# Performance work log

Hardware: AMD Instinct MI355X
Metric: run time of the kernel (lower is better)

Reference implementation:

```python
import jax, jax.numpy as jnp
import numpy as np
from jax import lax

EPS_BN = 1e-5
EPS_LN = 1e-5
K = 16  # patch size (cubic)
S = 8   # patch stride (cubic)


def _conv3d(x, w, stride):
    # x: [B,C,D,H,W], w: [O,I,kD,kH,kW], padding=1 on all spatial dims (torch padding=1)
    return lax.conv_general_dilated(
        x, w, (stride, stride, stride), [(1, 1), (1, 1), (1, 1)],
        dimension_numbers=('NCDHW', 'OIDHW', 'NCDHW'))


def _bn_relu(x, g, b):
    # train-mode BatchNorm3d: batch statistics over (B, D, H, W) per channel
    mean = jnp.mean(x, axis=(0, 2, 3, 4), keepdims=True)
    var = jnp.var(x, axis=(0, 2, 3, 4), keepdims=True)
    xh = (x - mean) * lax.rsqrt(var + EPS_BN)
    g = g[None, :, None, None, None]
    b = b[None, :, None, None, None]
    return jax.nn.relu(xh * g + b)


def _extract_patches_3d(f0):
    # f0: [B,C,D,H,W] -> patches [B,N,C*K^3] (C-major then kD,kH,kW, matching torch unfold),
    # coords [B,N,3]
    B, C, D, H, W = f0.shape
    Do, Ho, Wo = (D - K) // S + 1, (H - K) // S + 1, (W - K) // S + 1
    di = jnp.arange(Do)[:, None] * S + jnp.arange(K)[None, :]  # [Do,K]
    hi = jnp.arange(Ho)[:, None] * S + jnp.arange(K)[None, :]
    wi = jnp.arange(Wo)[:, None] * S + jnp.arange(K)[None, :]
    p = f0[:, :, di]                 # [B,C,Do,K,H,W]
    p = p[:, :, :, :, hi]            # [B,C,Do,K,Ho,K,W]
    p = p[:, :, :, :, :, :, wi]      # [B,C,Do,K,Ho,K,Wo,K]
    p = p.transpose(0, 2, 4, 6, 1, 3, 5, 7)  # [B,Do,Ho,Wo,C,K,K,K]
    patches = p.reshape(B, Do * Ho * Wo, C * K * K * K)
    half = (K - 1) / 2.0
    z = (jnp.arange(Do) * S + half) / max(D - 1, 1)
    y = (jnp.arange(Ho) * S + half) / max(H - 1, 1)
    xg = (jnp.arange(Wo) * S + half) / max(W - 1, 1)
    zz, yy, xx = jnp.meshgrid(z, y, xg, indexing='ij')
    coords = jnp.stack([zz.reshape(-1), yy.reshape(-1), xx.reshape(-1)], axis=-1)
    coords = jnp.broadcast_to(coords[None], (B,) + coords.shape)
    return patches, coords


def _layer_norm(x, g, b):
    mu = jnp.mean(x, axis=-1, keepdims=True)
    var = jnp.var(x, axis=-1, keepdims=True)
    return (x - mu) * lax.rsqrt(var + EPS_LN) * g + b


def setup_inputs() -> dict:
    key = jax.random.key(0)
    ks = jax.random.split(key, 8)
    C_in, mid, stem, tok_d, aux_d = 1, 16, 32, 128, 32
    pdim = stem * K * K * K  # 131072
    f32 = jnp.float32
    x = jax.random.normal(ks[0], (2, C_in, 128, 128, 128), dtype=f32)
    def kinit(k, shape, fan_in):
        return jax.random.normal(k, shape, dtype=f32) * (1.0 / np.sqrt(fan_in))
    return {
        'x': x,
        'conv1_w': kinit(ks[1], (mid, C_in, 3, 3, 3), C_in * 27),
        'bn1_g': jnp.ones((mid,), f32), 'bn1_b': jnp.zeros((mid,), f32),
        'conv2_w': kinit(ks[2], (mid, mid, 3, 3, 3), mid * 27),
        'bn2_g': jnp.ones((mid,), f32), 'bn2_b': jnp.zeros((mid,), f32),
        'conv3_w': kinit(ks[3], (stem, mid, 3, 3, 3), mid * 27),
        'bn3_g': jnp.ones((stem,), f32), 'bn3_b': jnp.zeros((stem,), f32),
        'tok_w': kinit(ks[4], (tok_d, pdim), pdim), 'tok_b': jnp.zeros((tok_d,), f32),
        'aux_w': kinit(ks[5], (aux_d, pdim), pdim), 'aux_b': jnp.zeros((aux_d,), f32),
        'ln_g': jnp.ones((tok_d,), f32), 'ln_b': jnp.zeros((tok_d,), f32),
    }


def reference(x, conv1_w, bn1_g, bn1_b, conv2_w, bn2_g, bn2_b, conv3_w, bn3_g, bn3_b,
              tok_w, tok_b, aux_w, aux_b, ln_g, ln_b):
    f0 = _bn_relu(_conv3d(x, conv1_w, 1), bn1_g, bn1_b)
    f0 = _bn_relu(_conv3d(f0, conv2_w, 1), bn2_g, bn2_b)
    f0 = _bn_relu(_conv3d(f0, conv3_w, 2), bn3_g, bn3_b)  # [B,32,64,64,64]
    patches, coords = _extract_patches_3d(f0)  # [B,N,131072]
    tokens = jnp.einsum('bnp,tp->bnt', patches, tok_w) + tok_b
    tokens = _layer_norm(tokens, ln_g, ln_b)
    aux = jnp.einsum('bnp,ap->bna', patches, aux_w) + aux_b
    return tokens, aux, coords
```

## Files before the change

### kernel.cpp

```cpp
#include <hip/hip_runtime.h>
#include <hip/hip_bf16.h>


typedef __hip_bfloat16 bf16;
typedef __attribute__((ext_vector_type(8))) short short8;
typedef __attribute__((ext_vector_type(4))) float f32x4;
__device__ __forceinline__ float b2f(bf16 v){ return __bfloat162float(v); }
__device__ __forceinline__ bf16 f2b(float v){ return __float2bfloat16(v); }
__device__ __forceinline__ unsigned short f2bu(float f){
  unsigned u = __float_as_uint(f);
  return (unsigned short)((u + 0x7fff + ((u>>16)&1)) >> 16);
}

#define SP12 2097152
#define SP3  262144
#define M_TOT 686
#define TOK_OFF 0
#define AUX_OFF 87808
#define CRD_OFF 109760
#define KSPLIT 32
#define NSLAB 32

__global__ __launch_bounds__(256) void k_packw(const float* __restrict__ w1,
                                               const float* __restrict__ w2,
                                               const float* __restrict__ w3,
                                               unsigned short* __restrict__ wp1,
                                               unsigned short* __restrict__ wp2,
                                               unsigned short* __restrict__ wp3){
  int i = blockIdx.x*256 + threadIdx.x;
  if(i < 512){
    int oc = i>>5, k = i&31;
    float v = (k<27)? w1[oc*27+k] : 0.f;
    wp1[i] = f2bu(v);
  } else if(i < 7680){
    int j = i - 512;
    int oc = j/448, k = j - oc*448;
    int tap = k>>4, ic = k&15;
    float v = (tap<27)? w2[(oc*16+ic)*27+tap] : 0.f;
    wp2[oc*448+k] = f2bu(v);
  } else if(i < 22016){
    int j = i - 7680;
    int oc = j/448, k = j - oc*448;
    int tap = k>>4, ic = k&15;
    float v = (tap<27)? w3[(oc*16+ic)*27+tap] : 0.f;
    wp3[oc*448+k] = f2bu(v);
  }
}

#define C1P 88
__global__ __launch_bounds__(256) void k_conv1(const float* __restrict__ x,
                                               const unsigned short* __restrict__ wp1,
                                               unsigned short* __restrict__ y1u,
                                               float* __restrict__ psum){
  __shared__ unsigned short in_l[6*6*C1P];
  int t = threadIdx.x;
  int bx = blockIdx.x;
  int xt = bx&1, yt = (bx>>1)&31, zt = (bx>>6)&31, b = bx>>11;
  int x0 = xt*64, y0 = yt*4, z0 = zt*4;

  for(int i=t; i<648; i+=256){
    int c = i%18; int row = i/18; int yy = row%6; int zz = row/6;
    int gz = z0-1+zz, gy = y0-1+yy;
    bool rowok = ((unsigned)gz<128u) && ((unsigned)gy<128u);
    int gx4 = x0-4+c*4;
    const float* rp = x + (size_t)b*SP12 + (rowok? ((gz<<14)+(gy<<7)) : 0);
    float v0,v1,v2,v3;
    if(rowok && gx4>=0 && gx4<=124){
      float4 v = *(const float4*)(rp + gx4);
      v0=v.x; v1=v.y; v2=v.z; v3=v.w;
    } else {
      float vv[4];
#pragma unroll
      for(int e=0;e<4;e++){
        int gx = gx4+e; bool ok = rowok && ((unsigned)gx<128u);
        float val = rp[ok? gx : 0];
        vv[e] = ok? val : 0.f;
      }
      v0=vv[0]; v1=vv[1]; v2=vv[2]; v3=vv[3];
    }
    uint2 p;
    p.x = (unsigned)f2bu(v0) | ((unsigned)f2bu(v1)<<16);
    p.y = (unsigned)f2bu(v2) | ((unsigned)f2bu(v3)<<16);
    *(uint2*)&in_l[row*C1P + c*4] = p;
  }
  __syncthreads();

  int lane = t&63, w = t>>6;
  int m = lane&15, q = lane>>4;
  short8 bfr = *(const short8*)(wp1 + m*32 + q*8);
  int toff[8];
#pragma unroll
  for(int j=0;j<8;j++){
    int tap = q*8+j; if(tap>26) tap=26;
    int dz = tap/9; int rr = tap-dz*9; int dy = rr/3; int dx = rr-dy*3;
    toff[j] = (dz*6+dy)*C1P + dx + 3 + m;
  }
  float s=0.f, qv=0.f;
#pragma unroll
  for(int yi=0; yi<4; yi++){
#pragma unroll
    for(int mg=0; mg<4; mg++){
      int base = (w*6+yi)*C1P + mg*16;
      short8 af;
#pragma unroll
      for(int j=0;j<8;j++) af[j] = (short)in_l[base + toff[j]];
      f32x4 acc = (f32x4){0.f,0.f,0.f,0.f};
      acc = __builtin_amdgcn_mfma_f32_16x16x32_bf16(af, bfr, acc, 0,0,0);
      int gz = z0+w, gy = y0+yi, gxb = x0 + mg*16 + q*4;
      size_t vbase = (size_t)((b<<21)|(gz<<14)|(gy<<7)|gxb);
      unsigned short* dst = y1u + vbase*16 + m;
#pragma unroll
      for(int reg=0; reg<4; reg++){
        float v = acc[reg];
        s += v; qv += v*v;
        dst[reg*16] = f2bu(v);
      }
    }
  }
  s  += __shfl_xor(s,16);  s  += __shfl_xor(s,32);
  qv += __shfl_xor(qv,16); qv += __shfl_xor(qv,32);
  __syncthreads();
  float* red = (float*)in_l;
  if(lane<16){ red[w*32+lane]=s; red[w*32+16+lane]=qv; }
  __syncthreads();
  if(t<32){
    float tot = red[t]+red[32+t]+red[64+t]+red[96+t];
    atomicAdd(&psum[(blockIdx.x & (NSLAB-1))*64 + t], tot);
  }
}

__global__ void k_finalize(const float* __restrict__ psum, const float* __restrict__ g,
                           const float* __restrict__ bb, float* __restrict__ scsh,
                           int C, float invN){
  int i = threadIdx.x;
  if(i<C){
    float s=0.f, q=0.f;
    for(int sl=0; sl<NSLAB; sl++){ s += psum[sl*64+i]; q += psum[sl*64+C+i]; }
    float mean = s*invN;
    float var  = q*invN - mean*mean;
    float sc = g[i]*rsqrtf(var+1e-5f);
    scsh[i]   = sc;
    scsh[C+i] = bb[i] - mean*sc;
  }
}

__global__ __launch_bounds__(256) void k_conv2(const unsigned short* __restrict__ y1u,
                                               const unsigned short* __restrict__ wp2,
                                               const float* __restrict__ scsh,
                                               unsigned short* __restrict__ y2u,
                                               float* __restrict__ psum2){
  __shared__ unsigned short tile[10*6*18*16];
  __shared__ float s_sc[16], s_sh[16];
  int t = threadIdx.x;
  if(t < 32){ float v = scsh[t]; if(t<16) s_sc[t]=v; else s_sh[t-16]=v; }
  __syncthreads();
  int bx = blockIdx.x;
  int txx = bx&7, tyy=(bx>>3)&31, tzz=(bx>>8)&15, b=bx>>12;
  int x0 = txx*16, y0 = tyy*4, z0 = tzz*8;
  for(int i=t;i<2160;i+=256){
    int vox = i>>1, h = i&1;
    int xl_ = vox%18; int r1 = vox/18; int yy_ = r1%6; int zz_ = r1/6;
    int gx = x0+xl_-1, gy = y0+yy_-1, gz = z0+zz_-1;
    bool ok = ((unsigned)gx<128u)&&((unsigned)gy<128u)&&((unsigned)gz<128u);
    uint4 o; o.x=0;o.y=0;o.z=0;o.w=0;
    if(ok){
      uint4 u = *(const uint4*)(y1u + ((size_t)((b<<21)|(gz<<14)|(gy<<7)|gx))*16 + h*8);
      int c0 = h*8;
      unsigned uu[4]; uu[0]=u.x; uu[1]=u.y; uu[2]=u.z; uu[3]=u.w;
      unsigned oo[4];
#pragma unroll
      for(int j=0;j<4;j++){
        float lo = fmaxf(__uint_as_float(uu[j]<<16)        *s_sc[c0+2*j]   + s_sh[c0+2*j],   0.f);
        float hi = fmaxf(__uint_as_float(uu[j]&0xffff0000u)*s_sc[c0+2*j+1] + s_sh[c0+2*j+1], 0.f);
        oo[j] = (unsigned)f2bu(lo) | ((unsigned)f2bu(hi)<<16);
      }
      o.x=oo[0]; o.y=oo[1]; o.z=oo[2]; o.w=oo[3];
    }
    int sw = (xl_>>2)&1;
    *(uint4*)&tile[vox*16 + ((h^sw)*8)] = o;
  }
  __syncthreads();

  int lane = t & 63, wid = t>>6;
  int m = lane & 15, q = lane>>4;
  int qh = q&1, qt = q>>1;
  f32x4 acc[8];
#pragma unroll
  for(int r=0;r<8;r++) acc[r] = (f32x4){0.f,0.f,0.f,0.f};
  const char* tbase = (const char*)tile + wid*6912;
  const unsigned short* wrow = wp2 + m*448 + q*8;
#pragma unroll
  for(int kp=0;kp<14;kp++){
    short8 bfr = *(const short8*)(wrow + kp*32);
    int tap = kp*2 + qt; if(tap>26) tap=26;
    int dz = tap/9; int rr = tap - dz*9; int dy = rr/3; int dx = rr - dy*3;
    int xl = m + dx;
    int abyte = ((dz*6 + dy)*18 + xl)*32 + ((qh ^ ((xl>>2)&1))*16);
    const char* ap = tbase + abyte;
#pragma unroll
    for(int r=0;r<8;r++){
      const short8 af = *(const short8*)(ap + ((r>>2)*6 + (r&3))*576);
      acc[r] = __builtin_amdgcn_mfma_f32_16x16x32_bf16(af, bfr, acc[r], 0,0,0);
    }
  }
  float s=0.f, qv=0.f;
#pragma unroll
  for(int r=0;r<8;r++){
    int gz = z0 + wid*2 + (r>>2), gy = y0 + (r&3);
    size_t vbase = (size_t)((b<<21)|(gz<<14)|(gy<<7)) + x0 + q*4;
#pragma unroll
    for(int reg=0;reg<4;reg++){
      float v = acc[r][reg];
      s += v; qv += v*v;
      y2u[(vbase+reg)*16 + m] = f2bu(v);
    }
  }
  s  += __shfl_xor(s,16);  s  += __shfl_xor(s,32);
  qv += __shfl_xor(qv,16); qv += __shfl_xor(qv,32);
  __syncthreads();
  float* red = (float*)tile;
  if(lane<16){ red[wid*32+lane]=s; red[wid*32+16+lane]=qv; }
  __syncthreads();
  if(t<32){
    float tot = red[t]+red[32+t]+red[64+t]+red[96+t];
    atomicAdd(&psum2[(blockIdx.x & (NSLAB-1))*64 + t], tot);
  }
}

__global__ __launch_bounds__(256) void k_conv3(const unsigned short* __restrict__ y2u,
                                               const unsigned short* __restrict__ wp3,
                                               const float* __restrict__ scsh,
                                               bf16* __restrict__ f0,
                                               float* __restrict__ psum3){
  __shared__ unsigned short tile3[5*9*33*16];
  __shared__ float s_sc[16], s_sh[16];
  int t = threadIdx.x;
  if(t < 32){ float v = scsh[t]; if(t<16) s_sc[t]=v; else s_sh[t-16]=v; }
  __syncthreads();
  int bx = blockIdx.x;
  int tx = bx&3, ty=(bx>>2)&15, tz=(bx>>6)&31, b=bx>>11;
  int x0 = tx*16, y0 = ty*4, z0 = tz*2;
  int gx0 = 2*x0-1, gy0 = 2*y0-1, gz0 = 2*z0-1;
  for(int i=t;i<2970;i+=256){
    int vox = i>>1, h = i&1;
    int xl_ = vox%33; int r1 = vox/33; int yy_ = r1%9; int zz_ = r1/9;
    int gx = gx0+xl_, gy = gy0+yy_, gz = gz0+zz_;
    bool ok = (gx>=0)&&(gy>=0)&&(gz>=0);
    uint4 o; o.x=0;o.y=0;o.z=0;o.w=0;
    if(ok){
      uint4 u = *(const uint4*)(y2u + ((size_t)((b<<21)|(gz<<14)|(gy<<7)|gx))*16 + h*8);
      int c0 = h*8;
      unsigned uu[4]; uu[0]=u.x; uu[1]=u.y; uu[2]=u.z; uu[3]=u.w;
      unsigned oo[4];
#pragma unroll
      for(int j=0;j<4;j++){
        float lo = fmaxf(__uint_as_float(uu[j]<<16)        *s_sc[c0+2*j]   + s_sh[c0+2*j],   0.f);
        float hi = fmaxf(__uint_as_float(uu[j]&0xffff0000u)*s_sc[c0+2*j+1] + s_sh[c0+2*j+1], 0.f);
        oo[j] = (unsigned)f2bu(lo) | ((unsigned)f2bu(hi)<<16);
      }
      o.x=oo[0]; o.y=oo[1]; o.z=oo[2]; o.w=oo[3];
    }
    int sw = (xl_>>2)&1;
    *(uint4*)&tile3[vox*16 + ((h^sw)*8)] = o;
  }
  __syncthreads();

  int lane = t & 63, wid = t>>6;
  int m = lane & 15, q = lane>>4;
  int qh = q&1, qt = q>>1;
  f32x4 acc[2][2];
#pragma unroll
  for(int r=0;r<2;r++){ acc[r][0]=(f32x4){0,0,0,0}; acc[r][1]=(f32x4){0,0,0,0}; }
  const unsigned short* wrow0 = wp3 + m*448 + q*8;
  const unsigned short* wrow1 = wp3 + (16+m)*448 + q*8;
#pragma unroll
  for(int kp=0;kp<14;kp++){
    short8 bf0 = *(const short8*)(wrow0 + kp*32);
    short8 bf1 = *(const short8*)(wrow1 + kp*32);
    int tap = kp*2 + qt; if(tap>26) tap=26;
    int dz = tap/9; int rr = tap - dz*9; int dy = rr/3; int dx = rr - dy*3;
    int xl = 2*m + dx;
    int hb = (qh ^ ((xl>>2)&1))*16;
#pragma unroll
    for(int rl=0;rl<2;rl++){
      int row = wid*2 + rl;
      int tz_ = 2*(row>>2) + dz;
      int ty_ = 2*(row&3) + dy;
      const short8 af = *(const short8*)((const char*)tile3 + ((tz_*9+ty_)*33 + xl)*32 + hb);
      acc[rl][0] = __builtin_amdgcn_mfma_f32_16x16x32_bf16(af, bf0, acc[rl][0], 0,0,0);
      acc[rl][1] = __builtin_amdgcn_mfma_f32_16x16x32_bf16(af, bf1, acc[rl][1], 0,0,0);
    }
  }
  float s0=0.f,q0=0.f,s1=0.f,q1=0.f;
#pragma unroll
  for(int rl=0;rl<2;rl++){
    int row = wid*2 + rl;
    int oz = z0 + (row>>2), oy = y0 + (row&3);
    size_t sp = (size_t)oz*4096 + oy*64 + x0 + q*4;
#pragma unroll
    for(int oct=0;oct<2;oct++){
      int oc = oct*16 + m;
      bf16* dst = f0 + (size_t)(b*32+oc)*SP3 + sp;
#pragma unroll
      for(int reg=0;reg<4;reg++){
        float v = acc[rl][oct][reg];
        if(oct==0){ s0 += v; q0 += v*v; } else { s1 += v; q1 += v*v; }
        dst[reg] = f2b(v);
      }
    }
  }
  s0 += __shfl_xor(s0,16); s0 += __shfl_xor(s0,32);
  q0 += __shfl_xor(q0,16); q0 += __shfl_xor(q0,32);
  s1 += __shfl_xor(s1,16); s1 += __shfl_xor(s1,32);
  q1 += __shfl_xor(q1,16); q1 += __shfl_xor(q1,32);
  __syncthreads();
  float* red = (float*)tile3;
  if(lane<16){
    red[wid*64+lane]    = s0; red[wid*64+16+lane] = s1;
    red[wid*64+32+lane] = q0; red[wid*64+48+lane] = q1;
  }
  __syncthreads();
  if(t<64){
    float tot = red[t]+red[64+t]+red[128+t]+red[192+t];
    atomicAdd(&psum3[(blockIdx.x & (NSLAB-1))*64 + t], tot);
  }
}

__global__ __launch_bounds__(256) void k_cvtw(const float* __restrict__ tokw,
                                              const float* __restrict__ auxw,
                                              unsigned short* __restrict__ wb){
  int i = blockIdx.x*256 + threadIdx.x;
  int n = i >> 15;
  int g = i & 32767;
  const float* src = (n<128)? tokw + (size_t)n*131072 : auxw + (size_t)(n-128)*131072;
  float4 v = *(const float4*)(src + g*4);
  ushort4 o; o.x=f2bu(v.x); o.y=f2bu(v.y); o.z=f2bu(v.z); o.w=f2bu(v.w);
  *(ushort4*)(wb + (size_t)n*131072 + g*4) = o;
}

__global__ __launch_bounds__(256) void k_gemm(const bf16* __restrict__ f0,
                                              const unsigned short* __restrict__ wb,
                                              const float* __restrict__ scsh3,
                                              float* __restrict__ out_acc){
  __shared__ unsigned short Al[64*72];
  __shared__ unsigned short Wl[160*72];
  int mblk = blockIdx.x % 11; int ks = blockIdx.x / 11;
  int M0 = mblk*64;
  int c  = ks;
  float sc = scsh3[c], sh = scsh3[32+c];
  int t = threadIdx.x;
  int lane = t & 63; int wid = t >> 6;
  int wm = (wid & 1)*32; int wn = (wid >> 1)*80;
  f32x4 acc[2][5];
#pragma unroll
  for(int i=0;i<2;i++)
#pragma unroll
    for(int j=0;j<5;j++) acc[i][j] = (f32x4){0.f,0.f,0.f,0.f};

  int ky_off0 = (t&7)>>1, half0 = t&1;
  int m_a = t>>3;
  int mg1 = M0 + m_a;       if(mg1>685) mg1=685;
  int mg2 = M0 + m_a + 32;  if(mg2>685) mg2=685;
  int b1 = mg1/343, r1 = mg1%343;
  int b2 = mg2/343, r2 = mg2%343;
  int sp1 = ((r1/49)*8)*4096 + (((r1/7)%7)*8)*64 + (r1%7)*8;
  int sp2 = ((r2/49)*8)*4096 + (((r2/7)%7)*8)*64 + (r2%7)*8;
  const bf16* f0c1 = f0 + (size_t)(b1*32+c)*SP3;
  const bf16* f0c2 = f0 + (size_t)(b2*32+c)*SP3;

  for(int bk=0; bk<64; bk++){
    int kz = bk>>2; int kyb = (bk&3)*4;
    __syncthreads();
#pragma unroll
    for(int p=0;p<5;p++){
      int n = p*32 + (t>>3);
      int koff = (t&7)*8;
      uint4 v = *(const uint4*)(wb + (size_t)n*131072 + ks*4096 + bk*64 + koff);
      *(uint4*)&Wl[n*72 + koff] = v;
    }
    {
      int ky = kyb + ky_off0; int xo = half0*8;
      int ldso = ky_off0*16 + half0*8;
      uint4 u1 = *(const uint4*)(f0c1 + sp1 + kz*4096 + ky*64 + xo);
      uint4 u2 = *(const uint4*)(f0c2 + sp2 + kz*4096 + ky*64 + xo);
      unsigned uu[8]; uu[0]=u1.x; uu[1]=u1.y; uu[2]=u1.z; uu[3]=u1.w;
      uu[4]=u2.x; uu[5]=u2.y; uu[6]=u2.z; uu[7]=u2.w;
      unsigned outw[8];
#pragma unroll
      for(int qq=0;qq<8;qq++){
        float lo = fmaxf(__uint_as_float(uu[qq]<<16)*sc + sh, 0.f);
        float hi = fmaxf(__uint_as_float(uu[qq]&0xffff0000u)*sc + sh, 0.f);
        outw[qq] = (unsigned)f2bu(lo) | ((unsigned)f2bu(hi)<<16);
      }
      uint4 w1; w1.x=outw[0]; w1.y=outw[1]; w1.z=outw[2]; w1.w=outw[3];
      uint4 w2; w2.x=outw[4]; w2.y=outw[5]; w2.z=outw[6]; w2.w=outw[7];
      *(uint4*)&Al[m_a*72 + ldso] = w1;
      *(uint4*)&Al[(m_a+32)*72 + ldso] = w2;
    }
    __syncthreads();
#pragma unroll
    for(int kstep=0;kstep<2;kstep++){
      int ko = kstep*32 + (lane>>4)*8;
      short8 af[2], bfr[5];
#pragma unroll
      for(int mt=0;mt<2;mt++)
        af[mt] = *(const short8*)&Al[(wm + mt*16 + (lane&15))*72 + ko];
#pragma unroll
      for(int nt=0;nt<5;nt++)
        bfr[nt] = *(const short8*)&Wl[(wn + nt*16 + (lane&15))*72 + ko];
#pragma unroll
      for(int mt=0;mt<2;mt++)
#pragma unroll
        for(int nt=0;nt<5;nt++)
          acc[mt][nt] = __builtin_amdgcn_mfma_f32_16x16x32_bf16(af[mt], bfr[nt], acc[mt][nt], 0,0,0);
    }
  }
#pragma unroll
  for(int mt=0;mt<2;mt++){
    int mb = M0 + wm + mt*16 + (lane>>4)*4;
#pragma unroll
    for(int nt=0;nt<5;nt++){
      int n = wn + nt*16 + (lane&15);
#pragma unroll
      for(int reg=0;reg<4;reg++){
        int mm = mb + reg;
        if(mm < M_TOT)
          out_acc[((size_t)ks*M_TOT + mm)*160 + n] = acc[mt][nt][reg];
      }
    }
  }
}

__global__ __launch_bounds__(256) void k_final(const float* __restrict__ out_acc,
                                               const float* __restrict__ tok_b,
                                               const float* __restrict__ aux_b,
                                               const float* __restrict__ ln_g,
                                               const float* __restrict__ ln_b,
                                               float* __restrict__ out){
  int m = blockIdx.x;
  int n = threadIdx.x;
  __shared__ float sA[128], sB[128];
  float sum = 0.f;
  if(n < 160){
    for(int ks=0;ks<KSPLIT;ks++) sum += out_acc[((size_t)ks*M_TOT+m)*160 + n];
  }
  float tval = 0.f;
  if(n < 128){
    tval = sum + tok_b[n];
    sA[n] = tval; sB[n] = tval*tval;
  }
  __syncthreads();
  for(int s=64;s>0;s>>=1){
    if(n < s){ sA[n] += sA[n+s]; sB[n] += sB[n+s]; }
    __syncthreads();
  }
  float mean = sA[0]*(1.f/128.f);
  float var  = sB[0]*(1.f/128.f) - mean*mean;
  float rstd = rsqrtf(var + 1e-5f);
  if(n<128){
    out[TOK_OFF + (size_t)m*128 + n] = (tval-mean)*rstd*ln_g[n] + ln_b[n];
  } else if(n<160){
    out[AUX_OFF + (size_t)m*32 + (n-128)] = sum + aux_b[n-128];
  } else if(n<163){
    int j = n-160;
    int pn = m % 343;
    int nz = pn/49, ny=(pn/7)%7, nx=pn%7;
    int g = (j==0)? nz : (j==1)? ny : nx;
    out[CRD_OFF + (size_t)m*3 + j] = (g*8 + 7.5f)*(1.f/63.f);
  }
}

extern "C" void kernel_launch(void* const* d_in, const int* in_sizes, int n_in,
                              void* d_out, int out_size, void* d_ws, size_t ws_size,
                              hipStream_t stream){
  const float* x    = (const float*)d_in[0];
  const float* w1   = (const float*)d_in[1];
  const float* g1   = (const float*)d_in[2];
  const float* b1   = (const float*)d_in[3];
  const float* w2   = (const float*)d_in[4];
  const float* g2   = (const float*)d_in[5];
  const float* b2   = (const float*)d_in[6];
  const float* w3   = (const float*)d_in[7];
  const float* g3   = (const float*)d_in[8];
  const float* b3   = (const float*)d_in[9];
  const float* tokw = (const float*)d_in[10];
  const float* tokb = (const float*)d_in[11];
  const float* auxw = (const float*)d_in[12];
  const float* auxb = (const float*)d_in[13];
  const float* lng  = (const float*)d_in[14];
  const float* lnb  = (const float*)d_in[15];
  float* out = (float*)d_out;

  char* ws = (char*)d_ws;
  unsigned short* y1u = (unsigned short*)ws;
  unsigned short* y2u = (unsigned short*)(ws + 134217728);
  bf16*  f0      = (bf16*)ws;
  float* out_acc = (float*)(ws + 33554432);
  unsigned short* wbf = (unsigned short*)(ws + 67108864);
  float* stats   = (float*)d_out;
  float* psum1 = stats;        float* psum2 = stats+2048; float* psum3 = stats+4096;
  float* scsh1 = stats+6144;   float* scsh2 = stats+6208; float* scsh3 = stats+6272;
  unsigned short* wp2 = (unsigned short*)(stats + 8192);
  unsigned short* wp3 = (unsigned short*)(stats + 12288);
  unsigned short* wp1 = (unsigned short*)(stats + 20480);

  hipMemsetAsync(stats, 0, 6144*sizeof(float), stream);

  k_packw<<<86, 256, 0, stream>>>(w1, w2, w3, wp1, wp2, wp3);
  k_conv1<<<4096, 256, 0, stream>>>(x, wp1, y1u, psum1);
  k_finalize<<<1, 64, 0, stream>>>(psum1, g1, b1, scsh1, 16, 1.f/4194304.f);
  k_conv2<<<8192, 256, 0, stream>>>(y1u, wp2, scsh1, y2u, psum2);
  k_finalize<<<1, 64, 0, stream>>>(psum2, g2, b2, scsh2, 16, 1.f/4194304.f);
  k_conv3<<<4096, 256, 0, stream>>>(y2u, wp3, scsh2, f0, psum3);
  k_finalize<<<1, 64, 0, stream>>>(psum3, g3, b3, scsh3, 32, 1.f/524288.f);
  k_cvtw<<<20480, 256, 0, stream>>>(tokw, auxw, wbf);
  k_gemm<<<352, 256, 0, stream>>>(f0, wbf, scsh3, out_acc);
  k_final<<<686, 256, 0, stream>>>(out_acc, tokb, auxb, lng, lnb, out);
}
```

Before: 505.4 us.

## Use packed bf16 conversion, swap MFMA operands for vector stores, split conv3 channels

Replaces the software bf16 rounding with the hardware v_cvt_pk_bf16_f32 instruction throughout. In conv1 and conv2 the MFMA operands are swapped so each lane holds four consecutive channels of one voxel, which allows a single 8-byte store in place of four scattered 2-byte stores; the statistics reduction changes to match. Conv3 now stages its input tile in two channel halves with an XOR-swizzled layout and a reordered weight packing, halving shared memory at the cost of an extra barrier pass. The packed conversion rounds slightly differently for NaN and edge cases.

```diff
diff --git a/kernel.cpp b/kernel.cpp
--- a/kernel.cpp
+++ b/kernel.cpp
@@ -10,6 +10,11 @@
 __device__ __forceinline__ unsigned short f2bu(float f){
   unsigned u = __float_as_uint(f);
   return (unsigned short)((u + 0x7fff + ((u>>16)&1)) >> 16);
+}
+__device__ __forceinline__ unsigned cvtpk(float lo, float hi){
+  unsigned r;
+  asm("v_cvt_pk_bf16_f32 %0, %1, %2" : "=v"(r) : "v"(lo), "v"(hi));
+  return r;
 }
 
 #define SP12 2097152
@@ -40,10 +45,12 @@
     wp2[oc*448+k] = f2bu(v);
   } else if(i < 22016){
     int j = i - 7680;
-    int oc = j/448, k = j - oc*448;
-    int tap = k>>4, ic = k&15;
+    int oc = j/448, r = j - oc*448;
+    int h = r/224, k2 = r - h*224;
+    int tap = (k2>>5)*4 + ((k2>>3)&3);
+    int ic = h*8 + (k2&7);
     float v = (tap<27)? w3[(oc*16+ic)*27+tap] : 0.f;
-    wp3[oc*448+k] = f2bu(v);
+    wp3[oc*448 + h*224 + k2] = f2bu(v);
   }
 }
 
@@ -79,15 +86,15 @@
       v0=vv[0]; v1=vv[1]; v2=vv[2]; v3=vv[3];
     }
     uint2 p;
-    p.x = (unsigned)f2bu(v0) | ((unsigned)f2bu(v1)<<16);
-    p.y = (unsigned)f2bu(v2) | ((unsigned)f2bu(v3)<<16);
+    p.x = cvtpk(v0,v1);
+    p.y = cvtpk(v2,v3);
     *(uint2*)&in_l[row*C1P + c*4] = p;
   }
   __syncthreads();
 
-  int lane = t&63, w = t>>6;
+  int lane = t&63, wv = t>>6;
   int m = lane&15, q = lane>>4;
-  short8 bfr = *(const short8*)(wp1 + m*32 + q*8);
+  short8 wfr = *(const short8*)(wp1 + m*32 + q*8);
   int toff[8];
 #pragma unroll
   for(int j=0;j<8;j++){
@@ -95,33 +102,39 @@
     int dz = tap/9; int rr = tap-dz*9; int dy = rr/3; int dx = rr-dy*3;
     toff[j] = (dz*6+dy)*C1P + dx + 3 + m;
   }
-  float s=0.f, qv=0.f;
+  float s4[4]={0.f,0.f,0.f,0.f}, q4[4]={0.f,0.f,0.f,0.f};
 #pragma unroll
   for(int yi=0; yi<4; yi++){
 #pragma unroll
     for(int mg=0; mg<4; mg++){
-      int base = (w*6+yi)*C1P + mg*16;
-      short8 af;
-#pragma unroll
-      for(int j=0;j<8;j++) af[j] = (short)in_l[base + toff[j]];
+      int base = (wv*6+yi)*C1P + mg*16;
+      short8 vf;
+#pragma unroll
+      for(int j=0;j<8;j++) vf[j] = (short)in_l[base + toff[j]];
       f32x4 acc = (f32x4){0.f,0.f,0.f,0.f};
-      acc = __builtin_amdgcn_mfma_f32_16x16x32_bf16(af, bfr, acc, 0,0,0);
-      int gz = z0+w, gy = y0+yi, gxb = x0 + mg*16 + q*4;
-      size_t vbase = (size_t)((b<<21)|(gz<<14)|(gy<<7)|gxb);
-      unsigned short* dst = y1u + vbase*16 + m;
+      acc = __builtin_amdgcn_mfma_f32_16x16x32_bf16(wfr, vf, acc, 0,0,0);
+      int gz = z0+wv, gy = y0+yi, gxv = x0 + mg*16 + m;
+      size_t vbase = (size_t)((b<<21)|(gz<<14)|(gy<<7)|gxv);
+      uint2 pw; pw.x = cvtpk(acc[0],acc[1]); pw.y = cvtpk(acc[2],acc[3]);
+      *(uint2*)(y1u + vbase*16 + q*4) = pw;
 #pragma unroll
       for(int reg=0; reg<4; reg++){
         float v = acc[reg];
-        s += v; qv += v*v;
-        dst[reg*16] = f2bu(v);
-      }
-    }
-  }
-  s  += __shfl_xor(s,16);  s  += __shfl_xor(s,32);
-  qv += __shfl_xor(qv,16); qv += __shfl_xor(qv,32);
+        s4[reg] += v; q4[reg] += v*v;
+      }
+    }
+  }
+#pragma unroll
+  for(int off=1; off<16; off<<=1){
+#pragma unroll
+    for(int rg=0;rg<4;rg++){ s4[rg] += __shfl_xor(s4[rg],off); q4[rg] += __shfl_xor(q4[rg],off); }
+  }
   __syncthreads();
   float* red = (float*)in_l;
-  if(lane<16){ red[w*32+lane]=s; red[w*32+16+lane]=qv; }
+  if(m==0){
+#pragma unroll
+    for(int rg=0;rg<4;rg++){ red[wv*32 + q*4+rg] = s4[rg]; red[wv*32+16 + q*4+rg] = q4[rg]; }
+  }
   __syncthreads();
   if(t<32){
     float tot = red[t]+red[32+t]+red[64+t]+red[96+t];
@@ -172,7 +185,7 @@
       for(int j=0;j<4;j++){
         float lo = fmaxf(__uint_as_float(uu[j]<<16)        *s_sc[c0+2*j]   + s_sh[c0+2*j],   0.f);
         float hi = fmaxf(__uint_as_float(uu[j]&0xffff0000u)*s_sc[c0+2*j+1] + s_sh[c0+2*j+1], 0.f);
-        oo[j] = (unsigned)f2bu(lo) | ((unsigned)f2bu(hi)<<16);
+        oo[j] = cvtpk(lo, hi);
       }
       o.x=oo[0]; o.y=oo[1]; o.z=oo[2]; o.w=oo[3];
     }
@@ -191,7 +204,7 @@
   const unsigned short* wrow = wp2 + m*448 + q*8;
 #pragma unroll
   for(int kp=0;kp<14;kp++){
-    short8 bfr = *(const short8*)(wrow + kp*32);
+    short8 wf = *(const short8*)(wrow + kp*32);
     int tap = kp*2 + qt; if(tap>26) tap=26;
     int dz = tap/9; int rr = tap - dz*9; int dy = rr/3; int dx = rr - dy*3;
     int xl = m + dx;
@@ -199,27 +212,34 @@
     const char* ap = tbase + abyte;
 #pragma unroll
     for(int r=0;r<8;r++){
-      const short8 af = *(const short8*)(ap + ((r>>2)*6 + (r&3))*576);
-      acc[r] = __builtin_amdgcn_mfma_f32_16x16x32_bf16(af, bfr, acc[r], 0,0,0);
-    }
-  }
-  float s=0.f, qv=0.f;
+      const short8 vf = *(const short8*)(ap + ((r>>2)*6 + (r&3))*576);
+      acc[r] = __builtin_amdgcn_mfma_f32_16x16x32_bf16(wf, vf, acc[r], 0,0,0);
+    }
+  }
+  float s4[4]={0.f,0.f,0.f,0.f}, q4[4]={0.f,0.f,0.f,0.f};
 #pragma unroll
   for(int r=0;r<8;r++){
     int gz = z0 + wid*2 + (r>>2), gy = y0 + (r&3);
-    size_t vbase = (size_t)((b<<21)|(gz<<14)|(gy<<7)) + x0 + q*4;
+    size_t vbase = (size_t)((b<<21)|(gz<<14)|(gy<<7)|(x0+m));
+    uint2 pw; pw.x = cvtpk(acc[r][0],acc[r][1]); pw.y = cvtpk(acc[r][2],acc[r][3]);
+    *(uint2*)(y2u + vbase*16 + q*4) = pw;
 #pragma unroll
     for(int reg=0;reg<4;reg++){
       float v = acc[r][reg];
-      s += v; qv += v*v;
-      y2u[(vbase+reg)*16 + m] = f2bu(v);
-    }
-  }
-  s  += __shfl_xor(s,16);  s  += __shfl_xor(s,32);
-  qv += __shfl_xor(qv,16); qv += __shfl_xor(qv,32);
+      s4[reg] += v; q4[reg] += v*v;
+    }
+  }
+#pragma unroll
+  for(int off=1; off<16; off<<=1){
+#pragma unroll
+    for(int rg=0;rg<4;rg++){ s4[rg] += __shfl_xor(s4[rg],off); q4[rg] += __shfl_xor(q4[rg],off); }
+  }
   __syncthreads();
   float* red = (float*)tile;
-  if(lane<16){ red[wid*32+lane]=s; red[wid*32+16+lane]=qv; }
+  if(m==0){
+#pragma unroll
+    for(int rg=0;rg<4;rg++){ red[wid*32 + q*4+rg] = s4[rg]; red[wid*32+16 + q*4+rg] = q4[rg]; }
+  }
   __syncthreads();
   if(t<32){
     float tot = red[t]+red[32+t]+red[64+t]+red[96+t];
@@ -227,12 +247,13 @@
   }
 }
 
+#define C3PITCH 576
 __global__ __launch_bounds__(256) void k_conv3(const unsigned short* __restrict__ y2u,
                                                const unsigned short* __restrict__ wp3,
                                                const float* __restrict__ scsh,
                                                bf16* __restrict__ f0,
                                                float* __restrict__ psum3){
-  __shared__ unsigned short tile3[5*9*33*16];
+  __shared__ unsigned short tile3[45*288];
   __shared__ float s_sc[16], s_sh[16];
   int t = threadIdx.x;
   if(t < 32){ float v = scsh[t]; if(t<16) s_sc[t]=v; else s_sh[t-16]=v; }
@@ -241,56 +262,62 @@
   int tx = bx&3, ty=(bx>>2)&15, tz=(bx>>6)&31, b=bx>>11;
   int x0 = tx*16, y0 = ty*4, z0 = tz*2;
   int gx0 = 2*x0-1, gy0 = 2*y0-1, gz0 = 2*z0-1;
-  for(int i=t;i<2970;i+=256){
-    int vox = i>>1, h = i&1;
-    int xl_ = vox%33; int r1 = vox/33; int yy_ = r1%9; int zz_ = r1/9;
-    int gx = gx0+xl_, gy = gy0+yy_, gz = gz0+zz_;
-    bool ok = (gx>=0)&&(gy>=0)&&(gz>=0);
-    uint4 o; o.x=0;o.y=0;o.z=0;o.w=0;
-    if(ok){
-      uint4 u = *(const uint4*)(y2u + ((size_t)((b<<21)|(gz<<14)|(gy<<7)|gx))*16 + h*8);
-      int c0 = h*8;
-      unsigned uu[4]; uu[0]=u.x; uu[1]=u.y; uu[2]=u.z; uu[3]=u.w;
-      unsigned oo[4];
-#pragma unroll
-      for(int j=0;j<4;j++){
-        float lo = fmaxf(__uint_as_float(uu[j]<<16)        *s_sc[c0+2*j]   + s_sh[c0+2*j],   0.f);
-        float hi = fmaxf(__uint_as_float(uu[j]&0xffff0000u)*s_sc[c0+2*j+1] + s_sh[c0+2*j+1], 0.f);
-        oo[j] = (unsigned)f2bu(lo) | ((unsigned)f2bu(hi)<<16);
-      }
-      o.x=oo[0]; o.y=oo[1]; o.z=oo[2]; o.w=oo[3];
-    }
-    int sw = (xl_>>2)&1;
-    *(uint4*)&tile3[vox*16 + ((h^sw)*8)] = o;
-  }
-  __syncthreads();
 
   int lane = t & 63, wid = t>>6;
   int m = lane & 15, q = lane>>4;
-  int qh = q&1, qt = q>>1;
   f32x4 acc[2][2];
 #pragma unroll
   for(int r=0;r<2;r++){ acc[r][0]=(f32x4){0,0,0,0}; acc[r][1]=(f32x4){0,0,0,0}; }
-  const unsigned short* wrow0 = wp3 + m*448 + q*8;
-  const unsigned short* wrow1 = wp3 + (16+m)*448 + q*8;
-#pragma unroll
-  for(int kp=0;kp<14;kp++){
-    short8 bf0 = *(const short8*)(wrow0 + kp*32);
-    short8 bf1 = *(const short8*)(wrow1 + kp*32);
-    int tap = kp*2 + qt; if(tap>26) tap=26;
-    int dz = tap/9; int rr = tap - dz*9; int dy = rr/3; int dx = rr - dy*3;
-    int xl = 2*m + dx;
-    int hb = (qh ^ ((xl>>2)&1))*16;
-#pragma unroll
-    for(int rl=0;rl<2;rl++){
-      int row = wid*2 + rl;
-      int tz_ = 2*(row>>2) + dz;
-      int ty_ = 2*(row&3) + dy;
-      const short8 af = *(const short8*)((const char*)tile3 + ((tz_*9+ty_)*33 + xl)*32 + hb);
-      acc[rl][0] = __builtin_amdgcn_mfma_f32_16x16x32_bf16(af, bf0, acc[rl][0], 0,0,0);
-      acc[rl][1] = __builtin_amdgcn_mfma_f32_16x16x32_bf16(af, bf1, acc[rl][1], 0,0,0);
-    }
-  }
+  const unsigned short* wr0 = wp3 + m*448      + q*8;
+  const unsigned short* wr1 = wp3 + (16+m)*448 + q*8;
+
+  for(int half=0; half<2; half++){
+    for(int i=t;i<1485;i+=256){
+      int xl_ = i%33; int r1 = i/33; int yy_ = r1%9; int zz_ = r1/9;
+      int gx = gx0+xl_, gy = gy0+yy_, gz = gz0+zz_;
+      bool ok = (gx>=0)&&(gy>=0)&&(gz>=0);
+      uint4 o; o.x=0;o.y=0;o.z=0;o.w=0;
+      if(ok){
+        uint4 u = *(const uint4*)(y2u + ((size_t)((b<<21)|(gz<<14)|(gy<<7)|gx))*16 + half*8);
+        int c0 = half*8;
+        unsigned uu[4]; uu[0]=u.x; uu[1]=u.y; uu[2]=u.z; uu[3]=u.w;
+        unsigned oo[4];
+#pragma unroll
+        for(int j=0;j<4;j++){
+          float lo = fmaxf(__uint_as_float(uu[j]<<16)        *s_sc[c0+2*j]   + s_sh[c0+2*j],   0.f);
+          float hi = fmaxf(__uint_as_float(uu[j]&0xffff0000u)*s_sc[c0+2*j+1] + s_sh[c0+2*j+1], 0.f);
+          oo[j] = cvtpk(lo, hi);
+        }
+        o.x=oo[0]; o.y=oo[1]; o.z=oo[2]; o.w=oo[3];
+      }
+      int sb = (xl_<<4) ^ ((xl_&8)<<1) ^ ((xl_&16)<<1);
+      *(uint4*)((char*)tile3 + (zz_*9+yy_)*C3PITCH + sb) = o;
+    }
+    __syncthreads();
+
+    const unsigned short* w0h = wr0 + half*224;
+    const unsigned short* w1h = wr1 + half*224;
+#pragma unroll
+    for(int kp=0;kp<7;kp++){
+      short8 bf0 = *(const short8*)(w0h + kp*32);
+      short8 bf1 = *(const short8*)(w1h + kp*32);
+      int tap = kp*4 + q; if(tap>26) tap=26;
+      int dz = tap/9; int rr = tap - dz*9; int dy = rr/3; int dx = rr - dy*3;
+      int xl = 2*m + dx;
+      int sb = (xl<<4) ^ ((xl&8)<<1) ^ ((xl&16)<<1);
+#pragma unroll
+      for(int rl=0;rl<2;rl++){
+        int row = wid*2 + rl;
+        int tz_ = 2*(row>>2) + dz;
+        int ty_ = 2*(row&3) + dy;
+        const short8 af = *(const short8*)((const char*)tile3 + (tz_*9+ty_)*C3PITCH + sb);
+        acc[rl][0] = __builtin_amdgcn_mfma_f32_16x16x32_bf16(af, bf0, acc[rl][0], 0,0,0);
+        acc[rl][1] = __builtin_amdgcn_mfma_f32_16x16x32_bf16(af, bf1, acc[rl][1], 0,0,0);
+      }
+    }
+    __syncthreads();
+  }
+
   float s0=0.f,q0=0.f,s1=0.f,q1=0.f;
 #pragma unroll
   for(int rl=0;rl<2;rl++){
@@ -301,11 +328,13 @@
     for(int oct=0;oct<2;oct++){
       int oc = oct*16 + m;
       bf16* dst = f0 + (size_t)(b*32+oc)*SP3 + sp;
+      f32x4 a = acc[rl][oct];
+      uint2 pw; pw.x = cvtpk(a[0],a[1]); pw.y = cvtpk(a[2],a[3]);
+      *(uint2*)dst = pw;
 #pragma unroll
       for(int reg=0;reg<4;reg++){
-        float v = acc[rl][oct][reg];
+        float v = a[reg];
         if(oct==0){ s0 += v; q0 += v*v; } else { s1 += v; q1 += v*v; }
-        dst[reg] = f2b(v);
       }
     }
   }
@@ -334,8 +363,8 @@
   int g = i & 32767;
   const float* src = (n<128)? tokw + (size_t)n*131072 : auxw + (size_t)(n-128)*131072;
   float4 v = *(const float4*)(src + g*4);
-  ushort4 o; o.x=f2bu(v.x); o.y=f2bu(v.y); o.z=f2bu(v.z); o.w=f2bu(v.w);
-  *(ushort4*)(wb + (size_t)n*131072 + g*4) = o;
+  uint2 pw; pw.x = cvtpk(v.x, v.y); pw.y = cvtpk(v.z, v.w);
+  *(uint2*)(wb + (size_t)n*131072 + g*4) = pw;
 }
 
 __global__ __launch_bounds__(256) void k_gemm(const bf16* __restrict__ f0,
@@ -390,7 +419,7 @@
       for(int qq=0;qq<8;qq++){
         float lo = fmaxf(__uint_as_float(uu[qq]<<16)*sc + sh, 0.f);
         float hi = fmaxf(__uint_as_float(uu[qq]&0xffff0000u)*sc + sh, 0.f);
-        outw[qq] = (unsigned)f2bu(lo) | ((unsigned)f2bu(hi)<<16);
+        outw[qq] = cvtpk(lo, hi);
       }
       uint4 w1; w1.x=outw[0]; w1.y=outw[1]; w1.z=outw[2]; w1.w=outw[3];
       uint4 w2; w2.x=outw[4]; w2.y=outw[5]; w2.z=outw[6]; w2.w=outw[7];
```

Result: faster. 484.4 us (-4.1%).
